# Optimization experiments

Measured on AMD Instinct MI355X. Metric: run time of the kernel, lower is better.

## Reference

```python
import jax, jax.numpy as jnp
import numpy as np

C_IMG = 256
H, W = 256, 704
CH = [32, 64, 128]
N = [100000, 80000, 60000]
COUT = CH[2] + 3  # 131


def setup_inputs() -> dict:
    key = jax.random.key(0)
    ks = jax.random.split(key, 20)
    inp = {}
    inp["img_feat"] = jax.random.normal(ks[0], (C_IMG, H, W), jnp.float32)
    for i in range(3):
        inp[f"voxel_feat_{i}"] = jax.random.normal(ks[1 + i], (N[i], CH[i]), jnp.float32)
        inp[f"voxel_coord_{i}"] = jax.random.normal(ks[4 + i], (N[i], 3), jnp.float32)
        # unique (row, col) cells so overwrite-on-duplicate scatter is deterministic
        lin = jax.random.permutation(ks[7 + i], H * W)[: N[i]]
        rows = lin // W
        cols = lin % W
        # module expects (x, y); pts2img swaps to (y, x)
        inp[f"img_grid_{i}"] = jnp.stack([cols, rows], axis=1).astype(jnp.int32)

    def conv_params(k, cin, cout, ksz):
        kw, kb = jax.random.split(k)
        w = jax.random.normal(kw, (cout, cin, ksz, ksz), jnp.float32) / np.sqrt(cin * ksz * ksz).astype(np.float32)
        b = jax.random.normal(kb, (cout,), jnp.float32) * 0.01
        return w, b

    inp["rd0_w"], inp["rd0_b"] = conv_params(ks[10], CH[0] + 3, COUT, 1)
    inp["rd1_w"], inp["rd1_b"] = conv_params(ks[11], CH[1] + 3, COUT, 1)
    inp["rd2_w"], inp["rd2_b"] = conv_params(ks[12], COUT, COUT, 1)
    inp["rd3_w"], inp["rd3_b"] = conv_params(ks[13], C_IMG, 1, 1)
    inp["sp_w"], inp["sp_b"] = conv_params(ks[14], COUT, 1, 3)
    return inp


def pts2img(grid_xy, feat):
    # scatter [N, C] features into dense (H, W) image grid -> (C, H, W)
    rows = grid_xy[:, 1].astype(jnp.int32)
    cols = grid_xy[:, 0].astype(jnp.int32)
    dense = jnp.zeros((H + 1, W + 1, feat.shape[1]), feat.dtype)
    dense = dense.at[rows, cols].set(feat)
    return dense[:-1, :-1].transpose(2, 0, 1)


def conv1x1(x, w, b):
    # x: (Cin, H, W), w: (Cout, Cin, 1, 1)
    return jnp.einsum('oi,ihw->ohw', w[:, :, 0, 0], x) + b[:, None, None]


def conv3x3(x, w, b):
    y = jax.lax.conv_general_dilated(x[None], w, (1, 1), 'SAME',
                                     dimension_numbers=('NCHW', 'OIHW', 'NCHW'))[0]
    return y + b[:, None, None]


def reference(img_feat, voxel_feat_0, voxel_coord_0, img_grid_0,
              voxel_feat_1, voxel_coord_1, img_grid_1,
              voxel_feat_2, voxel_coord_2, img_grid_2,
              rd0_w, rd0_b, rd1_w, rd1_b, rd2_w, rd2_b,
              rd3_w, rd3_b, sp_w, sp_b):
    f0 = pts2img(img_grid_0, jnp.concatenate([voxel_feat_0, voxel_coord_0], axis=-1))
    f1 = pts2img(img_grid_1, jnp.concatenate([voxel_feat_1, voxel_coord_1], axis=-1))
    f2 = pts2img(img_grid_2, jnp.concatenate([voxel_feat_2, voxel_coord_2], axis=-1))
    pt_img = conv1x1(f0, rd0_w, rd0_b) + conv1x1(f1, rd1_w, rd1_b) + f2
    pt_img = conv1x1(pt_img, rd2_w, rd2_b)
    gated = conv1x1(img_feat, rd3_w, rd3_b)  # (1, H, W), broadcast over COUT
    fused = gated + pt_img
    attention = jax.nn.sigmoid(conv3x3(fused, sp_w, sp_b))  # (1, H, W)
    return img_feat * attention
```

## Files before the change

### kernel.cpp

```cpp
#include <hip/hip_runtime.h>

#define HDIM 256
#define WDIM 704
#define HW (HDIM * WDIM)
#define CIMG 256
#define COUT 131

__global__ void precompute_kernel(const float* __restrict__ rd0_w, const float* __restrict__ rd0_b,
                                  const float* __restrict__ rd1_w, const float* __restrict__ rd1_b,
                                  const float* __restrict__ rd2_w, const float* __restrict__ rd2_b,
                                  const float* __restrict__ sp_w,
                                  float* __restrict__ T, float* __restrict__ G0,
                                  float* __restrict__ G1, float* __restrict__ cbwg) {
    __shared__ float s_base2[COUT];
    __shared__ float s_T[9 * COUT];
    int t = threadIdx.x;
    for (int j = t; j < COUT; j += blockDim.x) {
        float acc = rd2_b[j];
        for (int c = 0; c < COUT; ++c) acc += rd2_w[j * COUT + c] * (rd0_b[c] + rd1_b[c]);
        s_base2[j] = acc;
    }
    for (int e = t; e < 9 * COUT; e += blockDim.x) {
        int k = e / COUT, c = e - k * COUT;
        float acc = 0.f;
        for (int j = 0; j < COUT; ++j) acc += sp_w[j * 9 + k] * rd2_w[j * COUT + c];
        s_T[e] = acc;
        T[e] = acc;
    }
    __syncthreads();
    for (int e = t; e < 9 * 35; e += blockDim.x) {
        int k = e / 35, i = e - k * 35;
        float acc = 0.f;
        for (int c = 0; c < COUT; ++c) acc += s_T[k * COUT + c] * rd0_w[c * 35 + i];
        G0[e] = acc;
    }
    for (int e = t; e < 9 * 67; e += blockDim.x) {
        int k = e / 67, i = e - k * 67;
        float acc = 0.f;
        for (int c = 0; c < COUT; ++c) acc += s_T[k * COUT + c] * rd1_w[c * 67 + i];
        G1[e] = acc;
    }
    if (t < 9) {
        float acc = 0.f, accw = 0.f;
        for (int j = 0; j < COUT; ++j) {
            acc += sp_w[j * 9 + t] * s_base2[j];
            accw += sp_w[j * 9 + t];
        }
        cbwg[t] = acc;
        cbwg[9 + t] = accw;
    }
}

__global__ void gated_kernel(const float* __restrict__ img, const float* __restrict__ rd3_w,
                             const float* __restrict__ rd3_b, float* __restrict__ gated) {
    int pix = blockIdx.x * blockDim.x + threadIdx.x;
    if (pix >= HW) return;
    float g = rd3_b[0];
#pragma unroll 8
    for (int c = 0; c < CIMG; ++c) g += rd3_w[c] * img[(size_t)c * HW + pix];
    gated[pix] = g;
}

__global__ void scatter_kernel(const float* __restrict__ feat, const float* __restrict__ coord,
                               const int* __restrict__ grid, const float* __restrict__ G,
                               float* __restrict__ L, int n, int C) {
    int gid = blockIdx.x * blockDim.x + threadIdx.x;
    int p = gid >> 4;
    int lane = gid & 15;
    if (p >= n) return;
    int D = C + 3;
    float part[9];
#pragma unroll
    for (int k = 0; k < 9; ++k) part[k] = 0.f;
    for (int i = lane; i < D; i += 16) {
        float x = (i < C) ? feat[(size_t)p * C + i] : coord[(size_t)p * 3 + (i - C)];
#pragma unroll
        for (int k = 0; k < 9; ++k) part[k] += G[k * D + i] * x;
    }
#pragma unroll
    for (int k = 0; k < 9; ++k) {
        float v = part[k];
        v += __shfl_xor(v, 1);
        v += __shfl_xor(v, 2);
        v += __shfl_xor(v, 4);
        v += __shfl_xor(v, 8);
        part[k] = v;
    }
    if (lane < 9) {
        int kh = lane / 3, kw = lane - kh * 3;
        int cx = grid[2 * p], cy = grid[2 * p + 1];
        int h = cy - (kh - 1), w = cx - (kw - 1);
        if (h >= 0 && h < HDIM && w >= 0 && w < WDIM)
            atomicAdd(&L[h * WDIM + w], part[lane]);
    }
}

__global__ void attention_kernel(const float* __restrict__ gated, const float* __restrict__ L,
                                 const float* __restrict__ cbwg, const float* __restrict__ sp_b,
                                 float* __restrict__ att) {
    int pix = blockIdx.x * blockDim.x + threadIdx.x;
    if (pix >= HW) return;
    int h = pix / WDIM, w = pix - h * WDIM;
    float lg = sp_b[0] + L[pix];
#pragma unroll
    for (int kh = 0; kh < 3; ++kh) {
        int nh = h + kh - 1;
        if (nh < 0 || nh >= HDIM) continue;
#pragma unroll
        for (int kw = 0; kw < 3; ++kw) {
            int nw = w + kw - 1;
            if (nw < 0 || nw >= WDIM) continue;
            int k = kh * 3 + kw;
            lg += cbwg[k] + cbwg[9 + k] * gated[nh * WDIM + nw];
        }
    }
    att[pix] = 1.f / (1.f + expf(-lg));
}

__global__ void mul_kernel(const float* __restrict__ img, const float* __restrict__ att,
                           float* __restrict__ out) {
    const size_t n4 = (size_t)CIMG * HW / 4;
    const size_t stride = (size_t)gridDim.x * blockDim.x;
    for (size_t i = (size_t)blockIdx.x * blockDim.x + threadIdx.x; i < n4; i += stride) {
        float4 v = reinterpret_cast<const float4*>(img)[i];
        size_t e = i * 4;
        int pix = (int)(e % HW);
        float4 a = reinterpret_cast<const float4*>(att)[pix >> 2];
        v.x *= a.x;
        v.y *= a.y;
        v.z *= a.z;
        v.w *= a.w;
        reinterpret_cast<float4*>(out)[i] = v;
    }
}

extern "C" void kernel_launch(void* const* d_in, const int* in_sizes, int n_in,
                              void* d_out, int out_size, void* d_ws, size_t ws_size,
                              hipStream_t stream) {
    const float* img   = (const float*)d_in[0];
    const float* vf0   = (const float*)d_in[1];
    const float* vc0   = (const float*)d_in[2];
    const int*   g0    = (const int*)d_in[3];
    const float* vf1   = (const float*)d_in[4];
    const float* vc1   = (const float*)d_in[5];
    const int*   g1    = (const int*)d_in[6];
    const float* vf2   = (const float*)d_in[7];
    const float* vc2   = (const float*)d_in[8];
    const int*   g2    = (const int*)d_in[9];
    const float* rd0_w = (const float*)d_in[10];
    const float* rd0_b = (const float*)d_in[11];
    const float* rd1_w = (const float*)d_in[12];
    const float* rd1_b = (const float*)d_in[13];
    const float* rd2_w = (const float*)d_in[14];
    const float* rd2_b = (const float*)d_in[15];
    const float* rd3_w = (const float*)d_in[16];
    const float* rd3_b = (const float*)d_in[17];
    const float* sp_w  = (const float*)d_in[18];
    const float* sp_b  = (const float*)d_in[19];
    float* out = (float*)d_out;

    const int n0 = in_sizes[3] / 2;
    const int n1 = in_sizes[6] / 2;
    const int n2 = in_sizes[9] / 2;

    float* ws    = (float*)d_ws;
    float* L     = ws;
    float* gated = ws + HW;
    float* att   = ws + 2 * HW;
    float* T     = ws + 3 * HW;
    float* G0    = T + 9 * COUT;
    float* G1    = G0 + 9 * 35;
    float* cbwg  = G1 + 9 * 67;

    hipMemsetAsync(L, 0, HW * sizeof(float), stream);
    precompute_kernel<<<1, 256, 0, stream>>>(rd0_w, rd0_b, rd1_w, rd1_b, rd2_w, rd2_b, sp_w,
                                             T, G0, G1, cbwg);
    gated_kernel<<<(HW + 255) / 256, 256, 0, stream>>>(img, rd3_w, rd3_b, gated);
    scatter_kernel<<<(n0 * 16 + 255) / 256, 256, 0, stream>>>(vf0, vc0, g0, G0, L, n0, 32);
    scatter_kernel<<<(n1 * 16 + 255) / 256, 256, 0, stream>>>(vf1, vc1, g1, G1, L, n1, 64);
    scatter_kernel<<<(n2 * 16 + 255) / 256, 256, 0, stream>>>(vf2, vc2, g2, T, L, n2, 128);
    attention_kernel<<<(HW + 255) / 256, 256, 0, stream>>>(gated, L, cbwg, sp_b, att);
    mul_kernel<<<2048, 256, 0, stream>>>(img, att, out);
}
```

Before: 565.6 us.

## Parallelize precompute, vectorize gated/mul kernels, replace atomics with per-tap planes

```diff
diff --git a/kernel.cpp b/kernel.cpp
--- a/kernel.cpp
+++ b/kernel.cpp
@@ -3,6 +3,7 @@
 #define HDIM 256
 #define WDIM 704
 #define HW (HDIM * WDIM)
+#define HW4 (HW / 4)
 #define CIMG 256
 #define COUT 131
 
@@ -12,58 +13,68 @@
                                   const float* __restrict__ sp_w,
                                   float* __restrict__ T, float* __restrict__ G0,
                                   float* __restrict__ G1, float* __restrict__ cbwg) {
-    __shared__ float s_base2[COUT];
-    __shared__ float s_T[9 * COUT];
     int t = threadIdx.x;
-    for (int j = t; j < COUT; j += blockDim.x) {
-        float acc = rd2_b[j];
-        for (int c = 0; c < COUT; ++c) acc += rd2_w[j * COUT + c] * (rd0_b[c] + rd1_b[c]);
-        s_base2[j] = acc;
-    }
-    for (int e = t; e < 9 * COUT; e += blockDim.x) {
-        int k = e / COUT, c = e - k * COUT;
-        float acc = 0.f;
-        for (int j = 0; j < COUT; ++j) acc += sp_w[j * 9 + k] * rd2_w[j * COUT + c];
-        s_T[e] = acc;
-        T[e] = acc;
-    }
-    __syncthreads();
-    for (int e = t; e < 9 * 35; e += blockDim.x) {
-        int k = e / 35, i = e - k * 35;
-        float acc = 0.f;
-        for (int c = 0; c < COUT; ++c) acc += s_T[k * COUT + c] * rd0_w[c * 35 + i];
-        G0[e] = acc;
-    }
-    for (int e = t; e < 9 * 67; e += blockDim.x) {
-        int k = e / 67, i = e - k * 67;
-        float acc = 0.f;
-        for (int c = 0; c < COUT; ++c) acc += s_T[k * COUT + c] * rd1_w[c * 67 + i];
-        G1[e] = acc;
-    }
-    if (t < 9) {
-        float acc = 0.f, accw = 0.f;
-        for (int j = 0; j < COUT; ++j) {
-            acc += sp_w[j * 9 + t] * s_base2[j];
-            accw += sp_w[j * 9 + t];
+    if (blockIdx.x == 0) {
+        __shared__ float s_base2[COUT];
+        for (int j = t; j < COUT; j += blockDim.x) {
+            float acc = rd2_b[j];
+            for (int c = 0; c < COUT; ++c) acc += rd2_w[j * COUT + c] * (rd0_b[c] + rd1_b[c]);
+            s_base2[j] = acc;
         }
-        cbwg[t] = acc;
-        cbwg[9 + t] = accw;
+        __syncthreads();
+        if (t < 9) {
+            float acc = 0.f, accw = 0.f;
+            for (int j = 0; j < COUT; ++j) {
+                acc += sp_w[j * 9 + t] * s_base2[j];
+                accw += sp_w[j * 9 + t];
+            }
+            cbwg[t] = acc;
+            cbwg[9 + t] = accw;
+        }
+    } else {
+        int k = blockIdx.x - 1;
+        __shared__ float s_Tk[COUT];
+        for (int c = t; c < COUT; c += blockDim.x) {
+            float acc = 0.f;
+            for (int j = 0; j < COUT; ++j) acc += sp_w[j * 9 + k] * rd2_w[j * COUT + c];
+            s_Tk[c] = acc;
+            T[k * COUT + c] = acc;
+        }
+        __syncthreads();
+        for (int i = t; i < 35; i += blockDim.x) {
+            float acc = 0.f;
+            for (int c = 0; c < COUT; ++c) acc += s_Tk[c] * rd0_w[c * 35 + i];
+            G0[k * 35 + i] = acc;
+        }
+        for (int i = t; i < 67; i += blockDim.x) {
+            float acc = 0.f;
+            for (int c = 0; c < COUT; ++c) acc += s_Tk[c] * rd1_w[c * 67 + i];
+            G1[k * 67 + i] = acc;
+        }
     }
 }
 
-__global__ void gated_kernel(const float* __restrict__ img, const float* __restrict__ rd3_w,
-                             const float* __restrict__ rd3_b, float* __restrict__ gated) {
-    int pix = blockIdx.x * blockDim.x + threadIdx.x;
-    if (pix >= HW) return;
-    float g = rd3_b[0];
+__global__ void gated_kernel(const float4* __restrict__ img4, const float* __restrict__ rd3_w,
+                             const float* __restrict__ rd3_b, float4* __restrict__ gated4) {
+    int i = blockIdx.x * blockDim.x + threadIdx.x;
+    if (i >= HW4) return;
+    float b = rd3_b[0];
+    float4 g = {b, b, b, b};
 #pragma unroll 8
-    for (int c = 0; c < CIMG; ++c) g += rd3_w[c] * img[(size_t)c * HW + pix];
-    gated[pix] = g;
+    for (int c = 0; c < CIMG; ++c) {
+        float w = rd3_w[c];
+        float4 v = img4[(size_t)c * HW4 + i];
+        g.x += w * v.x;
+        g.y += w * v.y;
+        g.z += w * v.z;
+        g.w += w * v.w;
+    }
+    gated4[i] = g;
 }
 
 __global__ void scatter_kernel(const float* __restrict__ feat, const float* __restrict__ coord,
                                const int* __restrict__ grid, const float* __restrict__ G,
-                               float* __restrict__ L, int n, int C) {
+                               float* __restrict__ R, int n, int C) {
     int gid = blockIdx.x * blockDim.x + threadIdx.x;
     int p = gid >> 4;
     int lane = gid & 15;
@@ -87,21 +98,19 @@
         part[k] = v;
     }
     if (lane < 9) {
-        int kh = lane / 3, kw = lane - kh * 3;
         int cx = grid[2 * p], cy = grid[2 * p + 1];
-        int h = cy - (kh - 1), w = cx - (kw - 1);
-        if (h >= 0 && h < HDIM && w >= 0 && w < WDIM)
-            atomicAdd(&L[h * WDIM + w], part[lane]);
+        int cell = cy * WDIM + cx;
+        R[lane * HW + cell] += part[lane];
     }
 }
 
-__global__ void attention_kernel(const float* __restrict__ gated, const float* __restrict__ L,
+__global__ void attention_kernel(const float* __restrict__ gated, const float* __restrict__ R,
                                  const float* __restrict__ cbwg, const float* __restrict__ sp_b,
                                  float* __restrict__ att) {
     int pix = blockIdx.x * blockDim.x + threadIdx.x;
     if (pix >= HW) return;
     int h = pix / WDIM, w = pix - h * WDIM;
-    float lg = sp_b[0] + L[pix];
+    float lg = sp_b[0];
 #pragma unroll
     for (int kh = 0; kh < 3; ++kh) {
         int nh = h + kh - 1;
@@ -111,26 +120,27 @@
             int nw = w + kw - 1;
             if (nw < 0 || nw >= WDIM) continue;
             int k = kh * 3 + kw;
-            lg += cbwg[k] + cbwg[9 + k] * gated[nh * WDIM + nw];
+            int n = nh * WDIM + nw;
+            lg += cbwg[k] + cbwg[9 + k] * gated[n] + R[k * HW + n];
         }
     }
     att[pix] = 1.f / (1.f + expf(-lg));
 }
 
-__global__ void mul_kernel(const float* __restrict__ img, const float* __restrict__ att,
-                           float* __restrict__ out) {
-    const size_t n4 = (size_t)CIMG * HW / 4;
-    const size_t stride = (size_t)gridDim.x * blockDim.x;
-    for (size_t i = (size_t)blockIdx.x * blockDim.x + threadIdx.x; i < n4; i += stride) {
-        float4 v = reinterpret_cast<const float4*>(img)[i];
-        size_t e = i * 4;
-        int pix = (int)(e % HW);
-        float4 a = reinterpret_cast<const float4*>(att)[pix >> 2];
+__global__ void mul_kernel(const float4* __restrict__ img4, const float4* __restrict__ att4,
+                           float4* __restrict__ out4) {
+    int i = blockIdx.x * blockDim.x + threadIdx.x;
+    if (i >= HW4) return;
+    float4 a = att4[i];
+#pragma unroll
+    for (int cc = 0; cc < 8; ++cc) {
+        size_t idx = (size_t)(blockIdx.y * 8 + cc) * HW4 + i;
+        float4 v = img4[idx];
         v.x *= a.x;
         v.y *= a.y;
         v.z *= a.z;
         v.w *= a.w;
-        reinterpret_cast<float4*>(out)[i] = v;
+        out4[idx] = v;
     }
 }
 
@@ -164,21 +174,23 @@
     const int n2 = in_sizes[9] / 2;
 
     float* ws    = (float*)d_ws;
-    float* L     = ws;
-    float* gated = ws + HW;
-    float* att   = ws + 2 * HW;
-    float* T     = ws + 3 * HW;
+    float* R     = ws;
+    float* gated = R + 9 * HW;
+    float* att   = gated + HW;
+    float* T     = att + HW;
     float* G0    = T + 9 * COUT;
     float* G1    = G0 + 9 * 35;
     float* cbwg  = G1 + 9 * 67;
 
-    hipMemsetAsync(L, 0, HW * sizeof(float), stream);
-    precompute_kernel<<<1, 256, 0, stream>>>(rd0_w, rd0_b, rd1_w, rd1_b, rd2_w, rd2_b, sp_w,
-                                             T, G0, G1, cbwg);
-    gated_kernel<<<(HW + 255) / 256, 256, 0, stream>>>(img, rd3_w, rd3_b, gated);
-    scatter_kernel<<<(n0 * 16 + 255) / 256, 256, 0, stream>>>(vf0, vc0, g0, G0, L, n0, 32);
-    scatter_kernel<<<(n1 * 16 + 255) / 256, 256, 0, stream>>>(vf1, vc1, g1, G1, L, n1, 64);
-    scatter_kernel<<<(n2 * 16 + 255) / 256, 256, 0, stream>>>(vf2, vc2, g2, T, L, n2, 128);
-    attention_kernel<<<(HW + 255) / 256, 256, 0, stream>>>(gated, L, cbwg, sp_b, att);
-    mul_kernel<<<2048, 256, 0, stream>>>(img, att, out);
+    hipMemsetAsync(R, 0, (size_t)9 * HW * sizeof(float), stream);
+    precompute_kernel<<<10, 256, 0, stream>>>(rd0_w, rd0_b, rd1_w, rd1_b, rd2_w, rd2_b, sp_w,
+                                              T, G0, G1, cbwg);
+    gated_kernel<<<(HW4 + 255) / 256, 256, 0, stream>>>(
+        (const float4*)img, rd3_w, rd3_b, (float4*)gated);
+    scatter_kernel<<<(n0 * 16 + 255) / 256, 256, 0, stream>>>(vf0, vc0, g0, G0, R, n0, 32);
+    scatter_kernel<<<(n1 * 16 + 255) / 256, 256, 0, stream>>>(vf1, vc1, g1, G1, R, n1, 64);
+    scatter_kernel<<<(n2 * 16 + 255) / 256, 256, 0, stream>>>(vf2, vc2, g2, T, R, n2, 128);
+    attention_kernel<<<(HW + 255) / 256, 256, 0, stream>>>(gated, R, cbwg, sp_b, att);
+    dim3 mgrid((HW4 + 255) / 256, CIMG / 8);
+    mul_kernel<<<mgrid, 256, 0, stream>>>((const float4*)img, (const float4*)att, (float4*)out);
 }
```

Result: faster. 551.7 us (-2.5%).
